# Kernel tuning notes

Hardware: AMD Instinct MI355X
Metric: run time of the kernel (lower is better)

## Reference

```python
import jax, jax.numpy as jnp
import numpy as np

N_NODES = 100000
N_EDGES = 640000
IN_FEATS = 128
OUT_FEATS = 128


def setup_inputs() -> dict:
    key = jax.random.key(0)
    k1, k2, k3, k4 = jax.random.split(key, 4)
    feature = jax.random.normal(k1, (N_NODES, IN_FEATS), dtype=jnp.float32)
    edge_index = jax.random.randint(k2, (2, N_EDGES), 0, N_NODES, dtype=jnp.int64)
    # Linear params (W stored as [in, out] so out = h @ W + b, same math as torch Linear)
    W = jax.random.normal(k3, (IN_FEATS, OUT_FEATS), dtype=jnp.float32) / np.sqrt(IN_FEATS)
    b = jax.random.normal(k4, (OUT_FEATS,), dtype=jnp.float32) * 0.01
    return {"feature": feature, "edge_index": edge_index, "W": W, "b": b}


def reference(feature, edge_index, W, b):
    src, dst = edge_index[0], edge_index[1]
    # copy_src: gather source-node features along edges -> [E, in]
    msgs = feature[src]
    # sum reduce at destination nodes -> [N, in]
    h = jax.ops.segment_sum(msgs, dst, num_segments=N_NODES)
    # post-aggregation linear
    return h @ W + b
```

## Files before the change

### kernel.cpp

```cpp
#include <hip/hip_runtime.h>

#define N_NODES 100000
#define N_EDGES 640000
#define FEATS   128
#define CAP     32

typedef __attribute__((ext_vector_type(8))) short short8;
typedef __attribute__((ext_vector_type(4))) float f32x4;

static __device__ __forceinline__ unsigned short f2bf(float f) {
  union { float f; unsigned u; } c; c.f = f;
  unsigned u = c.u + 0x7fffu + ((c.u >> 16) & 1u);
  return (unsigned short)(u >> 16);
}
static __device__ __forceinline__ float asf(unsigned u) {
  union { unsigned u; float f; } c; c.u = u;
  return c.f;
}

__global__ __launch_bounds__(256) void fused_prep(
    const float* __restrict__ feature, const float* __restrict__ W,
    const int* __restrict__ edge,
    unsigned short* __restrict__ feat_bf, unsigned short* __restrict__ WT,
    int* __restrict__ cnt, int* __restrict__ bucket) {
  int b  = blockIdx.x;
  int sg = b / 24;
  int r  = b - sg * 24;

  if (r < 8 && sg < 313) {
    int cls  = r;
    int base = sg * 2048;
    #pragma unroll
    for (int k = 0; k < 8; ++k) {
      int e = base + k * 256 + threadIdx.x;
      if (e < N_EDGES) {
        int d = edge[N_EDGES + e];
        if (((d >> 4) & 7) == cls) {
          int s = edge[e];
          int slot = atomicAdd(&cnt[d], 1);
          if (slot < CAP) bucket[slot * N_NODES + d] = s;
        }
      }
    }
  } else {
    int idx = (sg < 313) ? (sg * 16 + (r - 8)) : (5008 + (b - 7512));
    if (idx < 6250) {
      size_t g = (size_t)idx * 256 + threadIdx.x;
      const float4* s = (const float4*)feature + g * 2;
      float4 a = s[0], c = s[1];
      unsigned short o[8] = {f2bf(a.x), f2bf(a.y), f2bf(a.z), f2bf(a.w),
                             f2bf(c.x), f2bf(c.y), f2bf(c.z), f2bf(c.w)};
      *(short8*)(feat_bf + g * 8) = *(const short8*)o;
    } else {
      int g = (idx - 6250) * 256 + threadIdx.x;
      int k = g >> 7, n = g & 127;
      WT[n * 128 + k] = f2bf(W[g]);
    }
  }
}

__global__ __launch_bounds__(256) void aggregate_kernel(
    const unsigned short* __restrict__ feat,
    const int* __restrict__ cnt, const int* __restrict__ bucket,
    unsigned short* __restrict__ h) {
  int g    = blockIdx.x * 256 + threadIdx.x;
  int node = g >> 4;
  int lane = g & 15;
  int deg  = min(cnt[node], CAP);
  const int* eb = bucket + node;

  float a0 = 0.f, a1 = 0.f, a2 = 0.f, a3 = 0.f;
  float a4 = 0.f, a5 = 0.f, a6 = 0.f, a7 = 0.f;

  int i = 0;
  for (; i + 3 < deg; i += 4) {
    int s0 = eb[(size_t)(i + 0) * N_NODES];
    int s1 = eb[(size_t)(i + 1) * N_NODES];
    int s2 = eb[(size_t)(i + 2) * N_NODES];
    int s3 = eb[(size_t)(i + 3) * N_NODES];
    uint4 p0 = *(const uint4*)(feat + (size_t)s0 * FEATS + lane * 8);
    uint4 p1 = *(const uint4*)(feat + (size_t)s1 * FEATS + lane * 8);
    uint4 p2 = *(const uint4*)(feat + (size_t)s2 * FEATS + lane * 8);
    uint4 p3 = *(const uint4*)(feat + (size_t)s3 * FEATS + lane * 8);
    a0 += asf(p0.x << 16) + asf(p1.x << 16) + asf(p2.x << 16) + asf(p3.x << 16);
    a1 += asf(p0.x & 0xffff0000u) + asf(p1.x & 0xffff0000u) + asf(p2.x & 0xffff0000u) + asf(p3.x & 0xffff0000u);
    a2 += asf(p0.y << 16) + asf(p1.y << 16) + asf(p2.y << 16) + asf(p3.y << 16);
    a3 += asf(p0.y & 0xffff0000u) + asf(p1.y & 0xffff0000u) + asf(p2.y & 0xffff0000u) + asf(p3.y & 0xffff0000u);
    a4 += asf(p0.z << 16) + asf(p1.z << 16) + asf(p2.z << 16) + asf(p3.z << 16);
    a5 += asf(p0.z & 0xffff0000u) + asf(p1.z & 0xffff0000u) + asf(p2.z & 0xffff0000u) + asf(p3.z & 0xffff0000u);
    a6 += asf(p0.w << 16) + asf(p1.w << 16) + asf(p2.w << 16) + asf(p3.w << 16);
    a7 += asf(p0.w & 0xffff0000u) + asf(p1.w & 0xffff0000u) + asf(p2.w & 0xffff0000u) + asf(p3.w & 0xffff0000u);
  }
  for (; i < deg; ++i) {
    int s = eb[(size_t)i * N_NODES];
    uint4 p = *(const uint4*)(feat + (size_t)s * FEATS + lane * 8);
    a0 += asf(p.x << 16);
    a1 += asf(p.x & 0xffff0000u);
    a2 += asf(p.y << 16);
    a3 += asf(p.y & 0xffff0000u);
    a4 += asf(p.z << 16);
    a5 += asf(p.z & 0xffff0000u);
    a6 += asf(p.w << 16);
    a7 += asf(p.w & 0xffff0000u);
  }

  uint4 o;
  o.x = (unsigned)f2bf(a0) | ((unsigned)f2bf(a1) << 16);
  o.y = (unsigned)f2bf(a2) | ((unsigned)f2bf(a3) << 16);
  o.z = (unsigned)f2bf(a4) | ((unsigned)f2bf(a5) << 16);
  o.w = (unsigned)f2bf(a6) | ((unsigned)f2bf(a7) << 16);
  *(uint4*)(h + (size_t)node * FEATS + lane * 8) = o;
}


#define LDSK 136

__global__ __launch_bounds__(256) void gemm_mfma(
    const unsigned short* __restrict__ hbf,
    const unsigned short* __restrict__ WT,
    const float* __restrict__ bias,
    float* __restrict__ out) {
  __shared__ unsigned short WTs[128 * LDSK];

  #pragma unroll
  for (int i = 0; i < 8; ++i) {
    int c = threadIdx.x + i * 256;
    int n = c >> 4, j = c & 15;
    *(short8*)&WTs[n * LDSK + j * 8] = *(const short8*)(WT + n * 128 + j * 8);
  }
  __syncthreads();

  const int w    = threadIdx.x >> 6;
  const int lane = threadIdx.x & 63;
  const int ln15 = lane & 15;
  const int quad = lane >> 4;
  const int row_base = blockIdx.x * 128 + w * 32;

  f32x4 acc[2][8] = {};

  #pragma unroll
  for (int kb = 0; kb < 4; ++kb) {
    int kofs = kb * 32 + quad * 8;
    short8 a0 = *(const short8*)(hbf + (size_t)(row_base + ln15) * FEATS + kofs);
    short8 a1 = *(const short8*)(hbf + (size_t)(row_base + 16 + ln15) * FEATS + kofs);
    #pragma unroll
    for (int ct = 0; ct < 8; ++ct) {
      short8 b = *(const short8*)&WTs[(ct * 16 + ln15) * LDSK + kofs];
      acc[0][ct] = __builtin_amdgcn_mfma_f32_16x16x32_bf16(a0, b, acc[0][ct], 0, 0, 0);
      acc[1][ct] = __builtin_amdgcn_mfma_f32_16x16x32_bf16(a1, b, acc[1][ct], 0, 0, 0);
    }
  }

  #pragma unroll
  for (int t = 0; t < 2; ++t) {
    #pragma unroll
    for (int ct = 0; ct < 8; ++ct) {
      int col = ct * 16 + ln15;
      float bv = bias[col];
      #pragma unroll
      for (int r = 0; r < 4; ++r) {
        int row = row_base + t * 16 + quad * 4 + r;
        if (row < N_NODES)
          __builtin_nontemporal_store(acc[t][ct][r] + bv,
                                      &out[(size_t)row * FEATS + col]);
      }
    }
  }
}


extern "C" void kernel_launch(void* const* d_in, const int* in_sizes, int n_in,
                              void* d_out, int out_size, void* d_ws, size_t ws_size,
                              hipStream_t stream) {
  const float* feature = (const float*)d_in[0];
  const int*   edge    = (const int*)d_in[1];
  const float* W       = (const float*)d_in[2];
  const float* bias    = (const float*)d_in[3];
  float*       out     = (float*)d_out;

  char* ws = (char*)d_ws;
  int* cnt    = (int*)(ws);
  int* bucket = (int*)(ws + (1 << 20));
  unsigned short* WT      = (unsigned short*)(ws + (27 << 20));
  unsigned short* feat_bf = (unsigned short*)(ws + (28 << 20));
  unsigned short* h_bf    = (unsigned short*)(ws + (54 << 20));

  hipMemsetAsync(cnt, 0, N_NODES * sizeof(int), stream);

  fused_prep<<<8818, 256, 0, stream>>>(
      feature, W, edge, feat_bf, WT, cnt, bucket);

  aggregate_kernel<<<N_NODES * 16 / 256, 256, 0, stream>>>(
      feat_bf, cnt, bucket, h_bf);

  gemm_mfma<<<(N_NODES + 127) / 128, 256, 0, stream>>>(h_bf, WT, bias, out);
}
```

Before: 180.0 us.

## Apply linear transform before aggregation and fuse GEMM into prep kernel

Uses linearity to compute feature@W first, inside the bucketing/prep kernel, and stores the result as bf16. The gather then sums the transformed rows and adds the bias directly into the fp32 output, so the intermediate aggregated h buffer and the separate GEMM launch go away. Each GEMM block rebuilds the transposed bf16 W in LDS from fp32 with scalar stores, and rounding now happens after the matmul instead of before, which changes the numerics slightly. The per-row bf16 output stores from the GEMM are 2-byte scattered writes.

```diff
diff --git a/kernel.cpp b/kernel.cpp
--- a/kernel.cpp
+++ b/kernel.cpp
@@ -4,6 +4,7 @@
 #define N_EDGES 640000
 #define FEATS   128
 #define CAP     32
+#define LDSK    136
 
 typedef __attribute__((ext_vector_type(8))) short short8;
 typedef __attribute__((ext_vector_type(4))) float f32x4;
@@ -18,54 +19,103 @@
   return c.f;
 }
 
-__global__ __launch_bounds__(256) void fused_prep(
+__global__ __launch_bounds__(256) void prep_gemm(
     const float* __restrict__ feature, const float* __restrict__ W,
     const int* __restrict__ edge,
-    unsigned short* __restrict__ feat_bf, unsigned short* __restrict__ WT,
-    int* __restrict__ cnt, int* __restrict__ bucket) {
+    int* __restrict__ cnt, int* __restrict__ bucket,
+    unsigned short* __restrict__ g_bf) {
+  __shared__ unsigned short WTs[128 * LDSK];
+
   int b  = blockIdx.x;
-  int sg = b / 24;
-  int r  = b - sg * 24;
+  int sg = b >> 4;
+  int r  = b & 15;
 
-  if (r < 8 && sg < 313) {
-    int cls  = r;
+  if (r < 8) {
     int base = sg * 2048;
     #pragma unroll
     for (int k = 0; k < 8; ++k) {
       int e = base + k * 256 + threadIdx.x;
       if (e < N_EDGES) {
         int d = edge[N_EDGES + e];
-        if (((d >> 4) & 7) == cls) {
+        if (((d >> 4) & 7) == r) {
           int s = edge[e];
           int slot = atomicAdd(&cnt[d], 1);
           if (slot < CAP) bucket[slot * N_NODES + d] = s;
         }
       }
     }
-  } else {
-    int idx = (sg < 313) ? (sg * 16 + (r - 8)) : (5008 + (b - 7512));
-    if (idx < 6250) {
-      size_t g = (size_t)idx * 256 + threadIdx.x;
-      const float4* s = (const float4*)feature + g * 2;
-      float4 a = s[0], c = s[1];
-      unsigned short o[8] = {f2bf(a.x), f2bf(a.y), f2bf(a.z), f2bf(a.w),
-                             f2bf(c.x), f2bf(c.y), f2bf(c.z), f2bf(c.w)};
-      *(short8*)(feat_bf + g * 8) = *(const short8*)o;
-    } else {
-      int g = (idx - 6250) * 256 + threadIdx.x;
-      int k = g >> 7, n = g & 127;
-      WT[n * 128 + k] = f2bf(W[g]);
+    return;
+  }
+
+  int idx = (r - 8) * 313 + sg;
+  if (idx >= 782) return;
+
+  #pragma unroll
+  for (int i = 0; i < 16; ++i) {
+    int q = i * 256 + threadIdx.x;
+    float4 v = *((const float4*)W + q);
+    int k = (q * 4) >> 7, n = (q * 4) & 127;
+    WTs[(n + 0) * LDSK + k] = f2bf(v.x);
+    WTs[(n + 1) * LDSK + k] = f2bf(v.y);
+    WTs[(n + 2) * LDSK + k] = f2bf(v.z);
+    WTs[(n + 3) * LDSK + k] = f2bf(v.w);
+  }
+  __syncthreads();
+
+  const int w    = threadIdx.x >> 6;
+  const int lane = threadIdx.x & 63;
+  const int ln15 = lane & 15;
+  const int quad = lane >> 4;
+  const int row_base = idx * 128 + w * 32;
+
+  f32x4 acc[2][8] = {};
+
+  #pragma unroll
+  for (int kb = 0; kb < 4; ++kb) {
+    int kofs = kb * 32 + quad * 8;
+    int r0 = min(row_base + ln15,      N_NODES - 1);
+    int r1 = min(row_base + 16 + ln15, N_NODES - 1);
+    const float* p0 = feature + (size_t)r0 * FEATS + kofs;
+    const float* p1 = feature + (size_t)r1 * FEATS + kofs;
+    float4 x0 = *(const float4*)p0, x1 = *(const float4*)(p0 + 4);
+    float4 y0 = *(const float4*)p1, y1 = *(const float4*)(p1 + 4);
+    unsigned short ua[8] = {f2bf(x0.x), f2bf(x0.y), f2bf(x0.z), f2bf(x0.w),
+                            f2bf(x1.x), f2bf(x1.y), f2bf(x1.z), f2bf(x1.w)};
+    unsigned short ub[8] = {f2bf(y0.x), f2bf(y0.y), f2bf(y0.z), f2bf(y0.w),
+                            f2bf(y1.x), f2bf(y1.y), f2bf(y1.z), f2bf(y1.w)};
+    short8 a0 = *(const short8*)ua;
+    short8 a1 = *(const short8*)ub;
+    #pragma unroll
+    for (int ct = 0; ct < 8; ++ct) {
+      short8 bb = *(const short8*)&WTs[(ct * 16 + ln15) * LDSK + kofs];
+      acc[0][ct] = __builtin_amdgcn_mfma_f32_16x16x32_bf16(a0, bb, acc[0][ct], 0, 0, 0);
+      acc[1][ct] = __builtin_amdgcn_mfma_f32_16x16x32_bf16(a1, bb, acc[1][ct], 0, 0, 0);
+    }
+  }
+
+  #pragma unroll
+  for (int t = 0; t < 2; ++t) {
+    #pragma unroll
+    for (int ct = 0; ct < 8; ++ct) {
+      int col = ct * 16 + ln15;
+      #pragma unroll
+      for (int rr = 0; rr < 4; ++rr) {
+        int row = row_base + t * 16 + quad * 4 + rr;
+        if (row < N_NODES)
+          g_bf[(size_t)row * FEATS + col] = f2bf(acc[t][ct][rr]);
+      }
     }
   }
 }
 
-__global__ __launch_bounds__(256) void aggregate_kernel(
-    const unsigned short* __restrict__ feat,
+__global__ __launch_bounds__(256) void gather_out(
+    const unsigned short* __restrict__ g,
     const int* __restrict__ cnt, const int* __restrict__ bucket,
-    unsigned short* __restrict__ h) {
-  int g    = blockIdx.x * 256 + threadIdx.x;
-  int node = g >> 4;
-  int lane = g & 15;
+    const float* __restrict__ bias,
+    float* __restrict__ out) {
+  int gi   = blockIdx.x * 256 + threadIdx.x;
+  int node = gi >> 4;
+  int lane = gi & 15;
   int deg  = min(cnt[node], CAP);
   const int* eb = bucket + node;
 
@@ -78,10 +128,10 @@
     int s1 = eb[(size_t)(i + 1) * N_NODES];
     int s2 = eb[(size_t)(i + 2) * N_NODES];
     int s3 = eb[(size_t)(i + 3) * N_NODES];
-    uint4 p0 = *(const uint4*)(feat + (size_t)s0 * FEATS + lane * 8);
-    uint4 p1 = *(const uint4*)(feat + (size_t)s1 * FEATS + lane * 8);
-    uint4 p2 = *(const uint4*)(feat + (size_t)s2 * FEATS + lane * 8);
-    uint4 p3 = *(const uint4*)(feat + (size_t)s3 * FEATS + lane * 8);
+    uint4 p0 = *(const uint4*)(g + (size_t)s0 * FEATS + lane * 8);
+    uint4 p1 = *(const uint4*)(g + (size_t)s1 * FEATS + lane * 8);
+    uint4 p2 = *(const uint4*)(g + (size_t)s2 * FEATS + lane * 8);
+    uint4 p3 = *(const uint4*)(g + (size_t)s3 * FEATS + lane * 8);
     a0 += asf(p0.x << 16) + asf(p1.x << 16) + asf(p2.x << 16) + asf(p3.x << 16);
     a1 += asf(p0.x & 0xffff0000u) + asf(p1.x & 0xffff0000u) + asf(p2.x & 0xffff0000u) + asf(p3.x & 0xffff0000u);
     a2 += asf(p0.y << 16) + asf(p1.y << 16) + asf(p2.y << 16) + asf(p3.y << 16);
@@ -93,7 +143,7 @@
   }
   for (; i < deg; ++i) {
     int s = eb[(size_t)i * N_NODES];
-    uint4 p = *(const uint4*)(feat + (size_t)s * FEATS + lane * 8);
+    uint4 p = *(const uint4*)(g + (size_t)s * FEATS + lane * 8);
     a0 += asf(p.x << 16);
     a1 += asf(p.x & 0xffff0000u);
     a2 += asf(p.y << 16);
@@ -104,68 +154,13 @@
     a7 += asf(p.w & 0xffff0000u);
   }
 
-  uint4 o;
-  o.x = (unsigned)f2bf(a0) | ((unsigned)f2bf(a1) << 16);
-  o.y = (unsigned)f2bf(a2) | ((unsigned)f2bf(a3) << 16);
-  o.z = (unsigned)f2bf(a4) | ((unsigned)f2bf(a5) << 16);
-  o.w = (unsigned)f2bf(a6) | ((unsigned)f2bf(a7) << 16);
-  *(uint4*)(h + (size_t)node * FEATS + lane * 8) = o;
-}
-
-
-#define LDSK 136
-
-__global__ __launch_bounds__(256) void gemm_mfma(
-    const unsigned short* __restrict__ hbf,
-    const unsigned short* __restrict__ WT,
-    const float* __restrict__ bias,
-    float* __restrict__ out) {
-  __shared__ unsigned short WTs[128 * LDSK];
-
-  #pragma unroll
-  for (int i = 0; i < 8; ++i) {
-    int c = threadIdx.x + i * 256;
-    int n = c >> 4, j = c & 15;
-    *(short8*)&WTs[n * LDSK + j * 8] = *(const short8*)(WT + n * 128 + j * 8);
-  }
-  __syncthreads();
-
-  const int w    = threadIdx.x >> 6;
-  const int lane = threadIdx.x & 63;
-  const int ln15 = lane & 15;
-  const int quad = lane >> 4;
-  const int row_base = blockIdx.x * 128 + w * 32;
-
-  f32x4 acc[2][8] = {};
-
-  #pragma unroll
-  for (int kb = 0; kb < 4; ++kb) {
-    int kofs = kb * 32 + quad * 8;
-    short8 a0 = *(const short8*)(hbf + (size_t)(row_base + ln15) * FEATS + kofs);
-    short8 a1 = *(const short8*)(hbf + (size_t)(row_base + 16 + ln15) * FEATS + kofs);
-    #pragma unroll
-    for (int ct = 0; ct < 8; ++ct) {
-      short8 b = *(const short8*)&WTs[(ct * 16 + ln15) * LDSK + kofs];
-      acc[0][ct] = __builtin_amdgcn_mfma_f32_16x16x32_bf16(a0, b, acc[0][ct], 0, 0, 0);
-      acc[1][ct] = __builtin_amdgcn_mfma_f32_16x16x32_bf16(a1, b, acc[1][ct], 0, 0, 0);
-    }
-  }
-
-  #pragma unroll
-  for (int t = 0; t < 2; ++t) {
-    #pragma unroll
-    for (int ct = 0; ct < 8; ++ct) {
-      int col = ct * 16 + ln15;
-      float bv = bias[col];
-      #pragma unroll
-      for (int r = 0; r < 4; ++r) {
-        int row = row_base + t * 16 + quad * 4 + r;
-        if (row < N_NODES)
-          __builtin_nontemporal_store(acc[t][ct][r] + bv,
-                                      &out[(size_t)row * FEATS + col]);
-      }
-    }
-  }
+  float4 b0 = *((const float4*)bias + lane * 2);
+  float4 b1 = *((const float4*)bias + lane * 2 + 1);
+  f32x4 o0 = {a0 + b0.x, a1 + b0.y, a2 + b0.z, a3 + b0.w};
+  f32x4 o1 = {a4 + b1.x, a5 + b1.y, a6 + b1.z, a7 + b1.w};
+  f32x4* dst = (f32x4*)(out + (size_t)node * FEATS + lane * 8);
+  __builtin_nontemporal_store(o0, dst);
+  __builtin_nontemporal_store(o1, dst + 1);
 }
 
 
@@ -181,17 +176,13 @@
   char* ws = (char*)d_ws;
   int* cnt    = (int*)(ws);
   int* bucket = (int*)(ws + (1 << 20));
-  unsigned short* WT      = (unsigned short*)(ws + (27 << 20));
-  unsigned short* feat_bf = (unsigned short*)(ws + (28 << 20));
-  unsigned short* h_bf    = (unsigned short*)(ws + (54 << 20));
+  unsigned short* g_bf = (unsigned short*)(ws + (28 << 20));
 
   hipMemsetAsync(cnt, 0, N_NODES * sizeof(int), stream);
 
-  fused_prep<<<8818, 256, 0, stream>>>(
-      feature, W, edge, feat_bf, WT, cnt, bucket);
+  prep_gemm<<<313 * 16, 256, 0, stream>>>(
+      feature, W, edge, cnt, bucket, g_bf);
 
-  aggregate_kernel<<<N_NODES * 16 / 256, 256, 0, stream>>>(
-      feat_bf, cnt, bucket, h_bf);
-
-  gemm_mfma<<<(N_NODES + 127) / 128, 256, 0, stream>>>(h_bf, WT, bias, out);
+  gather_out<<<N_NODES * 16 / 256, 256, 0, stream>>>(
+      g_bf, cnt, bucket, bias, out);
 }
```

Measured after the change: 249.0 us. 1.38x slower.
